# Performance work log

Measured on AMD Instinct MI355X. Metric: run time of the kernel, lower is better.

The kernel has to match this reference:

```python
import jax, jax.numpy as jnp
import numpy as np

FPS = [32, 64, 128, 256]
SPATIAL = [(32, 32, 32), (16, 16, 16), (8, 8, 8), (4, 4, 4)]
N_FEAT = 512
B = 2
HEAD_DIM = 16
EPS = 1e-5


def setup_inputs() -> dict:
    key = jax.random.key(0)
    ks = iter(jax.random.split(key, 64))
    inp = {}
    for i, (c, (h, w, z)) in enumerate(zip(FPS, SPATIAL)):
        inp[f"x{i}"] = jax.random.normal(next(ks), (B, c, h, w, z), jnp.float32)
        inp[f"f{i}"] = jax.random.normal(next(ks), (N_FEAT, c), jnp.float32)
        inp[f"kv_w{i}"] = jax.random.normal(next(ks), (2 * c, c), jnp.float32) * 0.02
        inp[f"kv_b{i}"] = jnp.zeros((2 * c,), jnp.float32)
        inp[f"proj_w{i}"] = jax.random.normal(next(ks), (c, c), jnp.float32) * 0.02
        inp[f"proj_b{i}"] = jnp.zeros((c,), jnp.float32)
        inp[f"ln_g{i}"] = jnp.ones((c,), jnp.float32)
        inp[f"ln_b{i}"] = jnp.zeros((c,), jnp.float32)
    inp["x4"] = jax.random.normal(next(ks), (B, 320, 2, 2, 2), jnp.float32)
    inp["x5"] = jax.random.normal(next(ks), (B, 320, 1, 1, 1), jnp.float32)
    return inp


def _block(x5d, feat, kv_w, kv_b, proj_w, proj_b, ln_g, ln_b):
    b, c, h, w, z = x5d.shape
    n = h * w * z
    H = c // HEAD_DIM
    # torch's x.view(b, h*w*z, c) is a raw reshape of [b,c,h,w,z] memory
    xq = x5d.reshape(b, n, c)
    N = feat.shape[0]
    f = jnp.broadcast_to(feat[None], (b, N, c))
    kv = f @ kv_w.T + kv_b                     # [b, N, 2c]
    kv = kv.reshape(b, N, 2, H, HEAD_DIM)
    k = kv[:, :, 0].transpose(0, 2, 1, 3)      # [b, H, N, hd]
    v = kv[:, :, 1].transpose(0, 2, 1, 3)      # [b, H, N, hd]
    q = xq.reshape(b, n, H, HEAD_DIM).transpose(0, 2, 1, 3) * (HEAD_DIM ** -0.5)
    attn = jax.nn.softmax(jnp.einsum('bhnd,bhmd->bhnm', q, k), axis=-1)
    o = jnp.einsum('bhnm,bhmd->bhnd', attn, v)
    o = o.transpose(0, 2, 1, 3).reshape(b, n, c)
    o = o @ proj_w.T + proj_b
    y = 0.5 * o + 0.5 * xq
    mu = jnp.mean(y, axis=-1, keepdims=True)
    var = jnp.var(y, axis=-1, keepdims=True)
    y = (y - mu) / jnp.sqrt(var + EPS) * ln_g + ln_b
    return y.reshape(b, c, h, w, z)


def reference(x0, x1, x2, x3, x4, x5, f0, f1, f2, f3,
              kv_w0, kv_b0, proj_w0, proj_b0, ln_g0, ln_b0,
              kv_w1, kv_b1, proj_w1, proj_b1, ln_g1, ln_b1,
              kv_w2, kv_b2, proj_w2, proj_b2, ln_g2, ln_b2,
              kv_w3, kv_b3, proj_w3, proj_b3, ln_g3, ln_b3):
    xs = [x0, x1, x2, x3]
    fs = [f0, f1, f2, f3]
    ps = [(kv_w0, kv_b0, proj_w0, proj_b0, ln_g0, ln_b0),
          (kv_w1, kv_b1, proj_w1, proj_b1, ln_g1, ln_b1),
          (kv_w2, kv_b2, proj_w2, proj_b2, ln_g2, ln_b2),
          (kv_w3, kv_b3, proj_w3, proj_b3, ln_g3, ln_b3)]
    res = [_block(xs[i], fs[i], *ps[i]) for i in range(4)]
    res.append(x4)  # stage 4: i >= 4 -> passthrough
    res.append(x5)  # last stage appended as-is
    return tuple(res)
```

## Files before the change

kernel.cpp:

```cpp
#include <hip/hip_runtime.h>

#define LOG2E 1.44269504088896340736f

typedef float v4f __attribute__((ext_vector_type(4)));

struct Params {
  const float* x[4]; const float* f[4]; const float* kvw[4]; const float* kvb[4];
  const float* pw[4]; const float* pb[4]; const float* g[4]; const float* lb[4];
  float* kb[4]; float* ob[4]; float* out[4];
};

__device__ inline v4f fmav(v4f a, v4f b, v4f c) { return a * b + c; }

__global__ __launch_bounds__(256) void kv_all(Params P) {
  int bid = blockIdx.x;
  int s, local;
  if (bid < 8)       { s = 0; local = bid; }
  else if (bid < 24) { s = 1; local = bid - 8; }
  else if (bid < 56) { s = 2; local = bid - 24; }
  else               { s = 3; local = bid - 56; }
  const int C = 32 << s;
  int nt = local & 7, jt = local >> 3;
  int n0 = nt * 64, j0 = jt * 64;
  const float* __restrict__ f = P.f[s];
  const float* __restrict__ w = P.kvw[s];
  __shared__ float fa[64][17];
  __shared__ float wb[64][17];
  int t = threadIdx.x;
  int ti = t & 15, tj = t >> 4;
  float acc[4][4];
  #pragma unroll
  for (int a = 0; a < 4; a++)
    #pragma unroll
    for (int b = 0; b < 4; b++) acc[a][b] = 0.f;

  for (int k0 = 0; k0 < C; k0 += 16) {
    __syncthreads();
    for (int i = t; i < 1024; i += 256) {
      int r = i >> 4, kk = i & 15;
      fa[r][kk] = f[(n0 + r) * C + k0 + kk];
      wb[r][kk] = w[(j0 + r) * C + k0 + kk];
    }
    __syncthreads();
    #pragma unroll
    for (int kk = 0; kk < 16; ++kk) {
      float av[4], bv[4];
      #pragma unroll
      for (int ii = 0; ii < 4; ii++) av[ii] = fa[ti * 4 + ii][kk];
      #pragma unroll
      for (int jj = 0; jj < 4; jj++) bv[jj] = wb[tj * 4 + jj][kk];
      #pragma unroll
      for (int ii = 0; ii < 4; ii++)
        #pragma unroll
        for (int jj = 0; jj < 4; jj++)
          acc[ii][jj] = fmaf(av[ii], bv[jj], acc[ii][jj]);
    }
  }
  const float* __restrict__ bias = P.kvb[s];
  float* kb = P.kb[s];
  #pragma unroll
  for (int ii = 0; ii < 4; ii++) {
    int n = n0 + ti * 4 + ii;
    #pragma unroll
    for (int jj = 0; jj < 4; jj++) {
      int j = j0 + tj * 4 + jj;
      float val = acc[ii][jj] + bias[j];
      if (j < C) {
        kb[(j >> 4) * 16384 + n * 32 + (j & 15)] = val;
      } else {
        int j2 = j - C;
        kb[(j2 >> 4) * 16384 + n * 32 + 16 + (j2 & 15)] = val;
      }
    }
  }
}

template <int C, int H>
__device__ void attn_stage(const Params& P, int s, int local, v4f* kvl) {
  constexpr int ROWS = 2 * ((C == 32) ? 32768 : (C == 64) ? 4096 : (C == 128) ? 512 : 64);
  int tile = local / H, head = local % H;
  const v4f* __restrict__ kvh = (const v4f*)(P.kb[s] + head * 16384);
  int t = threadIdx.x;
  int rowA = tile * 256 + t, rowB = rowA + 128;
  bool vA = rowA < ROWS, vB = rowB < ROWS;
  int rA = vA ? rowA : (ROWS - 1), rB = vB ? rowB : (ROWS - 1);

  const v4f* xa = (const v4f*)(P.x[s] + (size_t)rA * C + head * 16);
  const v4f* xb = (const v4f*)(P.x[s] + (size_t)rB * C + head * 16);
  const float qs = 0.25f * LOG2E;
  v4f qa0 = xa[0] * qs, qa1 = xa[1] * qs, qa2 = xa[2] * qs, qa3 = xa[3] * qs;
  v4f qb0 = xb[0] * qs, qb1 = xb[1] * qs, qb2 = xb[2] * qs, qb3 = xb[3] * qs;

  float ma = -1e30f, la = 0.f, mb = -1e30f, lb = 0.f;
  v4f aa0 = 0.f, aa1 = 0.f, aa2 = 0.f, aa3 = 0.f;
  v4f ab0 = 0.f, ab1 = 0.f, ab2 = 0.f, ab3 = 0.f;

  v4f pk[8];
  #pragma unroll
  for (int j = 0; j < 8; ++j) pk[j] = kvh[t + 128 * j];
  #pragma unroll
  for (int j = 0; j < 8; ++j) kvl[t + 128 * j] = pk[j];

  for (int c = 0; c < 4; ++c) {
    if (c < 3) {
      const v4f* src = kvh + (c + 1) * 1024;
      #pragma unroll
      for (int j = 0; j < 8; ++j) pk[j] = src[t + 128 * j];
    }
    __syncthreads();
    #pragma unroll 2
    for (int kl = 0; kl < 128; ++kl) {
      const v4f* row = kvl + kl * 8;
      v4f k0 = row[0], k1 = row[1], k2 = row[2], k3 = row[3];
      v4f ta = qa0 * k0; ta = fmav(qa1, k1, ta); ta = fmav(qa2, k2, ta); ta = fmav(qa3, k3, ta);
      v4f tb = qb0 * k0; tb = fmav(qb1, k1, tb); tb = fmav(qb2, k2, tb); tb = fmav(qb3, k3, tb);
      float sa = (ta.x + ta.y) + (ta.z + ta.w);
      float sb = (tb.x + tb.y) + (tb.z + tb.w);
      if (__any(fmaxf(sa - ma, sb - mb) > 8.f)) {
        float mna = fmaxf(ma, sa);
        float ra = __builtin_amdgcn_exp2f(ma - mna);
        la *= ra; aa0 *= ra; aa1 *= ra; aa2 *= ra; aa3 *= ra; ma = mna;
        float mnb = fmaxf(mb, sb);
        float rb = __builtin_amdgcn_exp2f(mb - mnb);
        lb *= rb; ab0 *= rb; ab1 *= rb; ab2 *= rb; ab3 *= rb; mb = mnb;
      }
      float pa = __builtin_amdgcn_exp2f(sa - ma);
      float pb = __builtin_amdgcn_exp2f(sb - mb);
      la += pa; lb += pb;
      v4f v0 = row[4], v1 = row[5], v2 = row[6], v3 = row[7];
      aa0 = fmav(pa, v0, aa0); aa1 = fmav(pa, v1, aa1);
      aa2 = fmav(pa, v2, aa2); aa3 = fmav(pa, v3, aa3);
      ab0 = fmav(pb, v0, ab0); ab1 = fmav(pb, v1, ab1);
      ab2 = fmav(pb, v2, ab2); ab3 = fmav(pb, v3, ab3);
    }
    __syncthreads();
    if (c < 3) {
      #pragma unroll
      for (int j = 0; j < 8; ++j) kvl[t + 128 * j] = pk[j];
    }
  }
  if (vA) {
    float inv = 1.f / la;
    v4f* o = (v4f*)(P.ob[s] + (size_t)rowA * C + head * 16);
    o[0] = aa0 * inv; o[1] = aa1 * inv; o[2] = aa2 * inv; o[3] = aa3 * inv;
  }
  if (vB) {
    float inv = 1.f / lb;
    v4f* o = (v4f*)(P.ob[s] + (size_t)rowB * C + head * 16);
    o[0] = ab0 * inv; o[1] = ab1 * inv; o[2] = ab2 * inv; o[3] = ab3 * inv;
  }
}

__global__ __launch_bounds__(128) void attn_all(Params P) {
  __shared__ v4f kvlds[1024];
  int bid = blockIdx.x;
  if (bid < 512)      attn_stage<32, 2>(P, 0, bid, kvlds);
  else if (bid < 640) attn_stage<64, 4>(P, 1, bid - 512, kvlds);
  else if (bid < 672) attn_stage<128, 8>(P, 2, bid - 640, kvlds);
  else                attn_stage<256, 16>(P, 3, bid - 672, kvlds);
}

__global__ __launch_bounds__(256) void copy_pass(const float4* __restrict__ x4,
                                                 const float4* __restrict__ x5,
                                                 float4* __restrict__ o) {
  int i = blockIdx.x * 256 + threadIdx.x;
  if (i < 1280)      o[i] = x4[i];
  else if (i < 1440) o[i] = x5[i - 1280];
}

template <int C>
__device__ void proj_stage(const Params& P, int s, int tile, float* olds) {
  constexpr int CP = C + 4;
  constexpr int R = 256 / C;
  constexpr int NR = 8;
  constexpr int RB = 2048 / C;
  int r0 = tile * RB;
  int t = threadIdx.x;
  const float4* __restrict__ obv = (const float4*)(P.ob[s] + (size_t)r0 * C);
  for (int i = t; i < 512; i += 256) {
    int row = i / (C / 4), kk = i % (C / 4);
    ((float4*)(olds + row * CP))[kk] = obv[i];
  }
  __syncthreads();
  int j = t % C, rg = t / C;
  const float* __restrict__ pw = P.pw[s];
  float acc[NR];
  #pragma unroll
  for (int i = 0; i < NR; ++i) acc[i] = 0.f;
  for (int k = 0; k < C; k += 4) {
    float4 w4 = *(const float4*)(pw + (size_t)j * C + k);
    #pragma unroll
    for (int i = 0; i < NR; ++i) {
      float4 o4 = *(const float4*)(olds + (rg + i * R) * CP + k);
      acc[i] = fmaf(o4.x, w4.x, acc[i]);
      acc[i] = fmaf(o4.y, w4.y, acc[i]);
      acc[i] = fmaf(o4.z, w4.z, acc[i]);
      acc[i] = fmaf(o4.w, w4.w, acc[i]);
    }
  }
  __syncthreads();
  float pbj = P.pb[s][j];
  const float* __restrict__ x = P.x[s];
  #pragma unroll
  for (int i = 0; i < NR; ++i) {
    int r = rg + i * R;
    float xv = x[(size_t)(r0 + r) * C + j];
    olds[r * CP + j] = 0.5f * (acc[i] + pbj) + 0.5f * xv;
  }
  __syncthreads();
  int lane = t & 63, wv = t >> 6;
  const float* __restrict__ g = P.g[s];
  const float* __restrict__ lb = P.lb[s];
  float* __restrict__ out = P.out[s];
  #pragma unroll
  for (int rr = 0; rr < RB / 4; ++rr) {
    int r = wv * (RB / 4) + rr;
    float sum = 0.f, sq = 0.f;
    #pragma unroll
    for (int ch = lane; ch < C; ch += 64) {
      float v = olds[r * CP + ch];
      sum += v; sq = fmaf(v, v, sq);
    }
    #pragma unroll
    for (int o = 32; o; o >>= 1) { sum += __shfl_xor(sum, o); sq += __shfl_xor(sq, o); }
    float mu = sum * (1.f / C);
    float var = sq * (1.f / C) - mu * mu;
    float rstd = rsqrtf(var + 1e-5f);
    #pragma unroll
    for (int ch = lane; ch < C; ch += 64) {
      float v = (olds[r * CP + ch] - mu) * rstd;
      out[(size_t)(r0 + r) * C + ch] = fmaf(v, g[ch], lb[ch]);
    }
  }
}

__global__ __launch_bounds__(256) void proj_ln_all(Params P) {
  __shared__ float olds[2304];
  int bid = blockIdx.x;
  if (bid < 1024)      proj_stage<32>(P, 0, bid, olds);
  else if (bid < 1280) proj_stage<64>(P, 1, bid - 1024, olds);
  else if (bid < 1344) proj_stage<128>(P, 2, bid - 1280, olds);
  else                 proj_stage<256>(P, 3, bid - 1344, olds);
}

extern "C" void kernel_launch(void* const* d_in, const int* in_sizes, int n_in,
                              void* d_out, int out_size, void* d_ws, size_t ws_size,
                              hipStream_t stream) {
  Params P;
  float* ws = (float*)d_ws;
  float* out = (float*)d_out;
  const size_t kvoff[4]  = {0, 32768, 98304, 229376};
  const size_t ooff[4]   = {491520, 2588672, 3112960, 3244032};
  const size_t outoff[4] = {0, 2097152, 2621440, 2752512};
  for (int i = 0; i < 4; ++i) {
    const int b = i * 8;
    P.x[i]   = (const float*)d_in[b + 0];
    P.f[i]   = (const float*)d_in[b + 1];
    P.kvw[i] = (const float*)d_in[b + 2];
    P.kvb[i] = (const float*)d_in[b + 3];
    P.pw[i]  = (const float*)d_in[b + 4];
    P.pb[i]  = (const float*)d_in[b + 5];
    P.g[i]   = (const float*)d_in[b + 6];
    P.lb[i]  = (const float*)d_in[b + 7];
    P.kb[i]  = ws + kvoff[i];
    P.ob[i]  = ws + ooff[i];
    P.out[i] = out + outoff[i];
  }

  copy_pass<<<6, 256, 0, stream>>>((const float4*)d_in[32], (const float4*)d_in[33],
                                   (float4*)(out + 2785280));
  kv_all<<<120, 256, 0, stream>>>(P);
  attn_all<<<688, 128, 0, stream>>>(P);
  proj_ln_all<<<1360, 256, 0, stream>>>(P);
}
```

Before: 318.4 us.

## Split attention over key groups with a separate log-sum-exp combine kernel

Attention now splits the 512 keys into G groups (4 when workspace allows) and launches 352*G blocks of 256 threads. Each block writes partial max, sum and accumulators, and a new combine kernel merges them. K/V are now read straight from global memory instead of being staged in LDS with double buffering. The attention output layout becomes head-major, so the projection loader gathers per head. The aim is more parallelism, at the cost of extra workspace traffic, an extra launch and uncached global K/V reads.

```diff
diff --git a/kernel.cpp b/kernel.cpp
--- a/kernel.cpp
+++ b/kernel.cpp
@@ -1,6 +1,7 @@
 #include <hip/hip_runtime.h>
 
 #define LOG2E 1.44269504088896340736f
+#define RHTOT 174080
 
 typedef float v4f __attribute__((ext_vector_type(4)));
 
@@ -75,89 +76,116 @@
   }
 }
 
-template <int C, int H>
-__device__ void attn_stage(const Params& P, int s, int local, v4f* kvl) {
-  constexpr int ROWS = 2 * ((C == 32) ? 32768 : (C == 64) ? 4096 : (C == 128) ? 512 : 64);
-  int tile = local / H, head = local % H;
-  const v4f* __restrict__ kvh = (const v4f*)(P.kb[s] + head * 16384);
+template <int C, int H, int ROWS, int RHB>
+__device__ void attn_stage(const float* __restrict__ kb, const float* __restrict__ x,
+                           float* __restrict__ accP, float* __restrict__ mP,
+                           float* __restrict__ lP, int local, int G, int KPG) {
+  int HG = H * G;
+  int tile = local / HG, r2 = local % HG;
+  int head = r2 / G, kg = r2 % G;
   int t = threadIdx.x;
-  int rowA = tile * 256 + t, rowB = rowA + 128;
-  bool vA = rowA < ROWS, vB = rowB < ROWS;
-  int rA = vA ? rowA : (ROWS - 1), rB = vB ? rowB : (ROWS - 1);
-
-  const v4f* xa = (const v4f*)(P.x[s] + (size_t)rA * C + head * 16);
-  const v4f* xb = (const v4f*)(P.x[s] + (size_t)rB * C + head * 16);
+  int row0 = tile * 512 + t;
+  if (row0 >= ROWS) return;
+  int row1 = row0 + 256;
+  bool v1 = row1 < ROWS;
+  int rc1 = v1 ? row1 : (ROWS - 1);
+  const float* __restrict__ kvh = kb + head * 16384 + (size_t)kg * KPG * 32;
+
   const float qs = 0.25f * LOG2E;
-  v4f qa0 = xa[0] * qs, qa1 = xa[1] * qs, qa2 = xa[2] * qs, qa3 = xa[3] * qs;
-  v4f qb0 = xb[0] * qs, qb1 = xb[1] * qs, qb2 = xb[2] * qs, qb3 = xb[3] * qs;
+  const v4f* xa = (const v4f*)(x + (size_t)row0 * C + head * 16);
+  const v4f* xb = (const v4f*)(x + (size_t)rc1 * C + head * 16);
+  v4f qa0 = xa[0]*qs, qa1 = xa[1]*qs, qa2 = xa[2]*qs, qa3 = xa[3]*qs;
+  v4f qb0 = xb[0]*qs, qb1 = xb[1]*qs, qb2 = xb[2]*qs, qb3 = xb[3]*qs;
 
   float ma = -1e30f, la = 0.f, mb = -1e30f, lb = 0.f;
   v4f aa0 = 0.f, aa1 = 0.f, aa2 = 0.f, aa3 = 0.f;
   v4f ab0 = 0.f, ab1 = 0.f, ab2 = 0.f, ab3 = 0.f;
 
-  v4f pk[8];
-  #pragma unroll
-  for (int j = 0; j < 8; ++j) pk[j] = kvh[t + 128 * j];
-  #pragma unroll
-  for (int j = 0; j < 8; ++j) kvl[t + 128 * j] = pk[j];
-
-  for (int c = 0; c < 4; ++c) {
-    if (c < 3) {
-      const v4f* src = kvh + (c + 1) * 1024;
-      #pragma unroll
-      for (int j = 0; j < 8; ++j) pk[j] = src[t + 128 * j];
-    }
-    __syncthreads();
-    #pragma unroll 2
-    for (int kl = 0; kl < 128; ++kl) {
-      const v4f* row = kvl + kl * 8;
-      v4f k0 = row[0], k1 = row[1], k2 = row[2], k3 = row[3];
-      v4f ta = qa0 * k0; ta = fmav(qa1, k1, ta); ta = fmav(qa2, k2, ta); ta = fmav(qa3, k3, ta);
-      v4f tb = qb0 * k0; tb = fmav(qb1, k1, tb); tb = fmav(qb2, k2, tb); tb = fmav(qb3, k3, tb);
-      float sa = (ta.x + ta.y) + (ta.z + ta.w);
-      float sb = (tb.x + tb.y) + (tb.z + tb.w);
-      if (__any(fmaxf(sa - ma, sb - mb) > 8.f)) {
-        float mna = fmaxf(ma, sa);
-        float ra = __builtin_amdgcn_exp2f(ma - mna);
-        la *= ra; aa0 *= ra; aa1 *= ra; aa2 *= ra; aa3 *= ra; ma = mna;
-        float mnb = fmaxf(mb, sb);
-        float rb = __builtin_amdgcn_exp2f(mb - mnb);
-        lb *= rb; ab0 *= rb; ab1 *= rb; ab2 *= rb; ab3 *= rb; mb = mnb;
-      }
-      float pa = __builtin_amdgcn_exp2f(sa - ma);
-      float pb = __builtin_amdgcn_exp2f(sb - mb);
-      la += pa; lb += pb;
-      v4f v0 = row[4], v1 = row[5], v2 = row[6], v3 = row[7];
-      aa0 = fmav(pa, v0, aa0); aa1 = fmav(pa, v1, aa1);
-      aa2 = fmav(pa, v2, aa2); aa3 = fmav(pa, v3, aa3);
-      ab0 = fmav(pb, v0, ab0); ab1 = fmav(pb, v1, ab1);
-      ab2 = fmav(pb, v2, ab2); ab3 = fmav(pb, v3, ab3);
-    }
-    __syncthreads();
-    if (c < 3) {
-      #pragma unroll
-      for (int j = 0; j < 8; ++j) kvl[t + 128 * j] = pk[j];
-    }
-  }
-  if (vA) {
+  #pragma unroll 2
+  for (int key = 0; key < KPG; ++key) {
+    const v4f* kr = (const v4f*)(kvh + (size_t)key * 32);
+    v4f k0 = kr[0], k1 = kr[1], k2 = kr[2], k3 = kr[3];
+    v4f ta = qa0 * k0; ta = fmav(qa1, k1, ta); ta = fmav(qa2, k2, ta); ta = fmav(qa3, k3, ta);
+    v4f tb = qb0 * k0; tb = fmav(qb1, k1, tb); tb = fmav(qb2, k2, tb); tb = fmav(qb3, k3, tb);
+    float sa = (ta.x + ta.y) + (ta.z + ta.w);
+    float sb = (tb.x + tb.y) + (tb.z + tb.w);
+    if (__any(fmaxf(sa - ma, sb - mb) > 8.f)) {
+      float mna = fmaxf(ma, sa);
+      float ra = __builtin_amdgcn_exp2f(ma - mna);
+      la *= ra; aa0 *= ra; aa1 *= ra; aa2 *= ra; aa3 *= ra; ma = mna;
+      float mnb = fmaxf(mb, sb);
+      float rb = __builtin_amdgcn_exp2f(mb - mnb);
+      lb *= rb; ab0 *= rb; ab1 *= rb; ab2 *= rb; ab3 *= rb; mb = mnb;
+    }
+    float pa = __builtin_amdgcn_exp2f(sa - ma);
+    float pb = __builtin_amdgcn_exp2f(sb - mb);
+    la += pa; lb += pb;
+    v4f v0 = kr[4], v1_ = kr[5], v2 = kr[6], v3 = kr[7];
+    aa0 = fmav(pa, v0, aa0); aa1 = fmav(pa, v1_, aa1);
+    aa2 = fmav(pa, v2, aa2); aa3 = fmav(pa, v3, aa3);
+    ab0 = fmav(pb, v0, ab0); ab1 = fmav(pb, v1_, ab1);
+    ab2 = fmav(pb, v2, ab2); ab3 = fmav(pb, v3, ab3);
+  }
+
+  size_t rhA = (size_t)RHB + (size_t)head * ROWS + row0;
+  size_t kgo = (size_t)kg * RHTOT;
+  if (G == 1) {
     float inv = 1.f / la;
-    v4f* o = (v4f*)(P.ob[s] + (size_t)rowA * C + head * 16);
-    o[0] = aa0 * inv; o[1] = aa1 * inv; o[2] = aa2 * inv; o[3] = aa3 * inv;
-  }
-  if (vB) {
-    float inv = 1.f / lb;
-    v4f* o = (v4f*)(P.ob[s] + (size_t)rowB * C + head * 16);
-    o[0] = ab0 * inv; o[1] = ab1 * inv; o[2] = ab2 * inv; o[3] = ab3 * inv;
-  }
-}
-
-__global__ __launch_bounds__(128) void attn_all(Params P) {
-  __shared__ v4f kvlds[1024];
+    v4f* d = (v4f*)(accP + rhA * 16);
+    d[0] = aa0 * inv; d[1] = aa1 * inv; d[2] = aa2 * inv; d[3] = aa3 * inv;
+    if (v1) {
+      float invb = 1.f / lb;
+      v4f* e = (v4f*)(accP + ((size_t)RHB + (size_t)head * ROWS + row1) * 16);
+      e[0] = ab0 * invb; e[1] = ab1 * invb; e[2] = ab2 * invb; e[3] = ab3 * invb;
+    }
+  } else {
+    mP[kgo + rhA] = ma; lP[kgo + rhA] = la;
+    v4f* d = (v4f*)(accP + (kgo + rhA) * 16);
+    d[0] = aa0; d[1] = aa1; d[2] = aa2; d[3] = aa3;
+    if (v1) {
+      size_t rhB = (size_t)RHB + (size_t)head * ROWS + row1;
+      mP[kgo + rhB] = mb; lP[kgo + rhB] = lb;
+      v4f* e = (v4f*)(accP + (kgo + rhB) * 16);
+      e[0] = ab0; e[1] = ab1; e[2] = ab2; e[3] = ab3;
+    }
+  }
+}
+
+__global__ __launch_bounds__(256) void attn_split(
+    const float* __restrict__ kb0, const float* __restrict__ kb1,
+    const float* __restrict__ kb2, const float* __restrict__ kb3,
+    const float* __restrict__ x0, const float* __restrict__ x1,
+    const float* __restrict__ x2, const float* __restrict__ x3,
+    float* __restrict__ accP, float* __restrict__ mP, float* __restrict__ lP,
+    int G, int KPG) {
   int bid = blockIdx.x;
-  if (bid < 512)      attn_stage<32, 2>(P, 0, bid, kvlds);
-  else if (bid < 640) attn_stage<64, 4>(P, 1, bid - 512, kvlds);
-  else if (bid < 672) attn_stage<128, 8>(P, 2, bid - 640, kvlds);
-  else                attn_stage<256, 16>(P, 3, bid - 672, kvlds);
+  int b0 = 256 * G, b1 = b0 + 64 * G, b2 = b1 + 16 * G;
+  if (bid < b0)      attn_stage<32, 2, 65536, 0>(kb0, x0, accP, mP, lP, bid, G, KPG);
+  else if (bid < b1) attn_stage<64, 4, 8192, 131072>(kb1, x1, accP, mP, lP, bid - b0, G, KPG);
+  else if (bid < b2) attn_stage<128, 8, 1024, 163840>(kb2, x2, accP, mP, lP, bid - b1, G, KPG);
+  else               attn_stage<256, 16, 128, 172032>(kb3, x3, accP, mP, lP, bid - b2, G, KPG);
+}
+
+__global__ __launch_bounds__(256) void combine_k(float* __restrict__ accP,
+                                                 const float* __restrict__ mP,
+                                                 const float* __restrict__ lP, int G) {
+  size_t rh = (size_t)blockIdx.x * 256 + threadIdx.x;
+  if (rh >= RHTOT) return;
+  float M = mP[rh];
+  for (int g = 1; g < G; ++g) M = fmaxf(M, mP[(size_t)g * RHTOT + rh]);
+  float lt = 0.f;
+  v4f o0 = 0.f, o1 = 0.f, o2 = 0.f, o3 = 0.f;
+  for (int g = 0; g < G; ++g) {
+    size_t idx = (size_t)g * RHTOT + rh;
+    float w = __builtin_amdgcn_exp2f(mP[idx] - M);
+    lt = fmaf(w, lP[idx], lt);
+    const v4f* a = (const v4f*)(accP + idx * 16);
+    o0 = fmav(w, a[0], o0); o1 = fmav(w, a[1], o1);
+    o2 = fmav(w, a[2], o2); o3 = fmav(w, a[3], o3);
+  }
+  float inv = 1.f / lt;
+  v4f* d = (v4f*)(accP + rh * 16);
+  d[0] = o0 * inv; d[1] = o1 * inv; d[2] = o2 * inv; d[3] = o3 * inv;
 }
 
 __global__ __launch_bounds__(256) void copy_pass(const float4* __restrict__ x4,
@@ -168,18 +196,21 @@
   else if (i < 1440) o[i] = x5[i - 1280];
 }
 
-template <int C>
+template <int C, int ROWS>
 __device__ void proj_stage(const Params& P, int s, int tile, float* olds) {
   constexpr int CP = C + 4;
   constexpr int R = 256 / C;
   constexpr int NR = 8;
   constexpr int RB = 2048 / C;
+  constexpr int RB4 = RB * 4;
   int r0 = tile * RB;
   int t = threadIdx.x;
-  const float4* __restrict__ obv = (const float4*)(P.ob[s] + (size_t)r0 * C);
+  const float4* __restrict__ ob4 = (const float4*)P.ob[s];
   for (int i = t; i < 512; i += 256) {
-    int row = i / (C / 4), kk = i % (C / 4);
-    ((float4*)(olds + row * CP))[kk] = obv[i];
+    int h = i / RB4, rem = i % RB4;
+    int row = rem >> 2, d4 = rem & 3;
+    float4 v = ob4[((size_t)h * ROWS + r0 + row) * 4 + d4];
+    ((float4*)(olds + row * CP + h * 16))[d4] = v;
   }
   __syncthreads();
   int j = t % C, rg = t / C;
@@ -237,10 +268,10 @@
 __global__ __launch_bounds__(256) void proj_ln_all(Params P) {
   __shared__ float olds[2304];
   int bid = blockIdx.x;
-  if (bid < 1024)      proj_stage<32>(P, 0, bid, olds);
-  else if (bid < 1280) proj_stage<64>(P, 1, bid - 1024, olds);
-  else if (bid < 1344) proj_stage<128>(P, 2, bid - 1280, olds);
-  else                 proj_stage<256>(P, 3, bid - 1344, olds);
+  if (bid < 1024)      proj_stage<32, 65536>(P, 0, bid, olds);
+  else if (bid < 1280) proj_stage<64, 8192>(P, 1, bid - 1024, olds);
+  else if (bid < 1344) proj_stage<128, 1024>(P, 2, bid - 1280, olds);
+  else                 proj_stage<256, 128>(P, 3, bid - 1344, olds);
 }
 
 extern "C" void kernel_launch(void* const* d_in, const int* in_sizes, int n_in,
@@ -250,8 +281,16 @@
   float* ws = (float*)d_ws;
   float* out = (float*)d_out;
   const size_t kvoff[4]  = {0, 32768, 98304, 229376};
-  const size_t ooff[4]   = {491520, 2588672, 3112960, 3244032};
+  const size_t A0 = 491520;
+  const size_t rhbase[4] = {0, 131072, 163840, 172032};
   const size_t outoff[4] = {0, 2097152, 2621440, 2752512};
+
+  int G = (ws_size >= (size_t)52101120) ? 4 : 1;
+  int KPG = 512 / G;
+  float* accP = ws + A0;
+  float* mP = accP + (size_t)G * 2785280;
+  float* lP = mP + (size_t)G * RHTOT;
+
   for (int i = 0; i < 4; ++i) {
     const int b = i * 8;
     P.x[i]   = (const float*)d_in[b + 0];
@@ -263,13 +302,16 @@
     P.g[i]   = (const float*)d_in[b + 6];
     P.lb[i]  = (const float*)d_in[b + 7];
     P.kb[i]  = ws + kvoff[i];
-    P.ob[i]  = ws + ooff[i];
+    P.ob[i]  = accP + rhbase[i] * 16;
     P.out[i] = out + outoff[i];
   }
 
   copy_pass<<<6, 256, 0, stream>>>((const float4*)d_in[32], (const float4*)d_in[33],
                                    (float4*)(out + 2785280));
   kv_all<<<120, 256, 0, stream>>>(P);
-  attn_all<<<688, 128, 0, stream>>>(P);
+  attn_split<<<352 * G, 256, 0, stream>>>(P.kb[0], P.kb[1], P.kb[2], P.kb[3],
+                                          P.x[0], P.x[1], P.x[2], P.x[3],
+                                          accP, mP, lP, G, KPG);
+  if (G > 1) combine_k<<<680, 256, 0, stream>>>(accP, mP, lP, G);
   proj_ln_all<<<1360, 256, 0, stream>>>(P);
 }
```

After: 357.3 us. 1.12x slower.
